# Performance work log

Hardware: AMD Instinct MI355X
Metric: run time of the kernel (lower is better)

Reference implementation:

```python
import jax, jax.numpy as jnp
import numpy as np

N, E, IN_DIM, EDGE_DIM, HID, OUT = 20000, 160000, 128, 32, 128, 64


def _p(key, shape):
    return jax.random.normal(key, shape, dtype=jnp.float32) * 0.05


def setup_inputs() -> dict:
    key = jax.random.key(0)
    ks = jax.random.split(key, 24)
    inp = {
        "x": jax.random.normal(ks[0], (N, IN_DIM), dtype=jnp.float32),
        "ei": jax.random.randint(ks[1], (2, E), 0, N, dtype=jnp.int64),
        "ea": jax.random.normal(ks[2], (E, EDGE_DIM), dtype=jnp.float32),
    }
    H1C1 = 4 * HID  # layer1: heads=4, out=HID, concat -> 512
    # layer 1 params (in=IN_DIM)
    inp["Wq1"] = _p(ks[3], (H1C1, IN_DIM)); inp["bq1"] = _p(ks[4], (H1C1,))
    inp["Wk1"] = _p(ks[5], (H1C1, IN_DIM)); inp["bk1"] = _p(ks[6], (H1C1,))
    inp["Wv1"] = _p(ks[7], (H1C1, IN_DIM)); inp["bv1"] = _p(ks[8], (H1C1,))
    inp["We1"] = _p(ks[9], (H1C1, EDGE_DIM))
    inp["Ws1"] = _p(ks[10], (H1C1, IN_DIM)); inp["bs1"] = _p(ks[11], (H1C1,))
    # layer 2 params (in=512, heads=1, out=OUT, concat=False)
    IN2 = H1C1
    inp["Wq2"] = _p(ks[12], (OUT, IN2)); inp["bq2"] = _p(ks[13], (OUT,))
    inp["Wk2"] = _p(ks[14], (OUT, IN2)); inp["bk2"] = _p(ks[15], (OUT,))
    inp["Wv2"] = _p(ks[16], (OUT, IN2)); inp["bv2"] = _p(ks[17], (OUT,))
    inp["We2"] = _p(ks[18], (OUT, EDGE_DIM))
    inp["Ws2"] = _p(ks[19], (OUT, IN2)); inp["bs2"] = _p(ks[20], (OUT,))
    return inp


def transformer_conv(x, ei, ea, Wq, bq, Wk, bk, Wv, bv, We, Ws, bs, heads, C, concat):
    """PyG TransformerConv: gather -> per-edge attention -> segment softmax -> scatter."""
    n = x.shape[0]
    src, dst = ei[0], ei[1]  # messages flow src -> dst
    q = (x @ Wq.T + bq).reshape(n, heads, C)
    k = (x @ Wk.T + bk).reshape(n, heads, C)
    v = (x @ Wv.T + bv).reshape(n, heads, C)
    e = (ea @ We.T).reshape(-1, heads, C)  # [E,H,C]
    kj = k[src] + e
    vj = v[src] + e
    alpha = jnp.einsum("ehc,ehc->eh", q[dst], kj) / jnp.sqrt(jnp.float32(C))
    # segment softmax over incoming edges of each dst node
    amax = jax.ops.segment_max(alpha, dst, num_segments=n)
    ex = jnp.exp(alpha - amax[dst])
    denom = jax.ops.segment_sum(ex, dst, num_segments=n)
    w = ex / denom[dst]  # [E,H]
    out = jax.ops.segment_sum(vj * w[:, :, None], dst, num_segments=n)  # [N,H,C]
    out = out.reshape(n, heads * C) if concat else out.mean(axis=1)
    return out + x @ Ws.T + bs  # root/skip connection


def reference(x, ei, ea,
              Wq1, bq1, Wk1, bk1, Wv1, bv1, We1, Ws1, bs1,
              Wq2, bq2, Wk2, bk2, Wv2, bv2, We2, Ws2, bs2):
    h = jax.nn.relu(transformer_conv(x, ei, ea, Wq1, bq1, Wk1, bk1, Wv1, bv1,
                                     We1, Ws1, bs1, heads=4, C=HID, concat=True))
    z = transformer_conv(h, ei, ea, Wq2, bq2, Wk2, bk2, Wv2, bv2,
                         We2, Ws2, bs2, heads=1, C=OUT, concat=False)
    return z
```

## Files before the change

### kernel.cpp

```cpp
#include <hip/hip_runtime.h>
#include <hip/hip_bf16.h>
#include <math.h>

#define N_NODES 20000
#define N_EDGES 160000
#define D1 512
#define D2 64
#define Y1W 2176
#define Y2W 288

typedef __attribute__((ext_vector_type(8))) short short8;
typedef __attribute__((ext_vector_type(4))) float floatx4;

__device__ __forceinline__ float bf2f(short u) {
    return __uint_as_float(((unsigned)(unsigned short)u) << 16);
}
__device__ __forceinline__ short f2bf(float f) {
    __hip_bfloat16 h = __float2bfloat16(f);
    return *(short*)&h;
}

__global__ void hist_kernel(const int* __restrict__ ei, int* __restrict__ deg) {
    int e = blockIdx.x * blockDim.x + threadIdx.x;
    if (e < N_EDGES) atomicAdd(&deg[ei[N_EDGES + e]], 1);
}

__global__ void scan_kernel(const int* __restrict__ deg, int* __restrict__ rowptr) {
    const int NT = 1024;
    const int CH = (N_NODES + NT - 1) / NT;
    __shared__ int sums[NT];
    int t = threadIdx.x;
    int base = t * CH;
    int s = 0;
    for (int i = 0; i < CH; ++i) {
        int idx = base + i;
        if (idx < N_NODES) s += deg[idx];
    }
    sums[t] = s;
    __syncthreads();
    for (int off = 1; off < NT; off <<= 1) {
        int v = (t >= off) ? sums[t - off] : 0;
        __syncthreads();
        sums[t] += v;
        __syncthreads();
    }
    int run = (t > 0) ? sums[t - 1] : 0;
    for (int i = 0; i < CH; ++i) {
        int idx = base + i;
        if (idx < N_NODES) {
            rowptr[idx] = run;
            run += deg[idx];
        }
    }
    if (t == NT - 1) rowptr[N_NODES] = sums[NT - 1];
}

__global__ void fill_kernel(const int* __restrict__ ei, const int* __restrict__ rowptr,
                            int* __restrict__ cursor, int* __restrict__ srcs,
                            int* __restrict__ eid) {
    int e = blockIdx.x * blockDim.x + threadIdx.x;
    if (e < N_EDGES) {
        int src = ei[e];
        int dst = ei[N_EDGES + e];
        int p = rowptr[dst] + atomicAdd(&cursor[dst], 1);
        srcs[p] = src;
        eid[p] = e;
    }
}

__global__ void eaperm_kernel(const float* __restrict__ ea, const int* __restrict__ eid,
                              float* __restrict__ eap) {
    int idx = blockIdx.x * 256 + threadIdx.x;
    if (idx >= N_EDGES * 32) return;
    int p = idx >> 5, d = idx & 31;
    eap[idx] = ea[(size_t)eid[p] * 32 + d];
}

__global__ void prep1_kernel(const float* __restrict__ Wq1, const float* __restrict__ bq1,
                             const float* __restrict__ Wk1, const float* __restrict__ bk1,
                             const float* __restrict__ Wv1, const float* __restrict__ bv1,
                             const float* __restrict__ Ws1, const float* __restrict__ bs1,
                             const float* __restrict__ We1,
                             __hip_bfloat16* __restrict__ W1b, float* __restrict__ b1) {
    int j = blockIdx.x, t = threadIdx.x;
    if (j < 2048) {
        int sel = j >> 9, r = j & 511;
        const float* W = sel == 0 ? Wq1 : sel == 1 ? Wk1 : sel == 2 ? Wv1 : Ws1;
        const float* bs = sel == 0 ? bq1 : sel == 1 ? bk1 : sel == 2 ? bv1 : bs1;
        W1b[(size_t)j * 128 + t] = __float2bfloat16(W[(size_t)r * 128 + t]);
        if (t == 0) b1[j] = bs[r];
    } else {
        int hd = j - 2048, h = hd >> 5, d = hd & 31;
        float acc = 0.f;
        for (int c = 0; c < 128; ++c)
            acc += Wq1[(size_t)(h * 128 + c) * 128 + t] * We1[(size_t)(h * 128 + c) * 32 + d];
        W1b[(size_t)j * 128 + t] = __float2bfloat16(acc);
        if (t == 0) {
            float b = 0.f;
            for (int c = 0; c < 128; ++c) b += bq1[h * 128 + c] * We1[(size_t)(h * 128 + c) * 32 + d];
            b1[j] = b;
        }
    }
}

__global__ void prep2_kernel(const float* __restrict__ Wq2, const float* __restrict__ bq2,
                             const float* __restrict__ Wk2, const float* __restrict__ bk2,
                             const float* __restrict__ Wv2, const float* __restrict__ bv2,
                             const float* __restrict__ Ws2, const float* __restrict__ bs2,
                             const float* __restrict__ We2,
                             __hip_bfloat16* __restrict__ W2b, float* __restrict__ b2) {
    int j = blockIdx.x, t = threadIdx.x;
    for (int kk = t; kk < 512; kk += 256) {
        float val;
        if (j < 256) {
            int sel = j >> 6, r = j & 63;
            const float* W = sel == 0 ? Wq2 : sel == 1 ? Wk2 : sel == 2 ? Wv2 : Ws2;
            val = W[(size_t)r * 512 + kk];
        } else {
            int d = j - 256;
            float acc = 0.f;
            for (int c = 0; c < 64; ++c) acc += Wq2[(size_t)c * 512 + kk] * We2[c * 32 + d];
            val = acc;
        }
        W2b[(size_t)j * 512 + kk] = __float2bfloat16(val);
    }
    if (t == 0) {
        if (j < 256) {
            int sel = j >> 6, r = j & 63;
            const float* bs = sel == 0 ? bq2 : sel == 1 ? bk2 : sel == 2 ? bv2 : bs2;
            b2[j] = bs[r];
        } else {
            int d = j - 256;
            float b = 0.f;
            for (int c = 0; c < 64; ++c) b += bq2[c] * We2[c * 32 + d];
            b2[j] = b;
        }
    }
}

template <int K, bool A_F32, bool OUT_BF16>
__global__ __launch_bounds__(256) void gemm_bt(const void* __restrict__ Ap,
                                               const __hip_bfloat16* __restrict__ B,
                                               const float* __restrict__ bias,
                                               void* __restrict__ Cout,
                                               int M, int N, int tiles_n) {
    __shared__ char lds[65536];
    char* ldsA = lds;
    char* ldsB = lds + 32768;
    int tid = threadIdx.x;
    int bm = blockIdx.x / tiles_n, bn = blockIdx.x % tiles_n;
    int w = tid >> 6, lane = tid & 63;
    int wr = (w >> 1) * 64, wc = (w & 1) * 64;
    int lrow = lane & 15, lk = lane >> 4;
    floatx4 acc[4][4] = {};

    for (int kt = 0; kt < K / 128; ++kt) {
        if (kt) __syncthreads();
        #pragma unroll
        for (int it = 0; it < 8; ++it) {
            int s = it * 256 + tid;
            int row = s >> 4, kslot = s & 15;
            int phys = ((kslot ^ (row & 15)) << 4);
            int gr = bm * 128 + row;
            if (gr > M - 1) gr = M - 1;
            short8 va;
            if (A_F32) {
                const float* Af = (const float*)Ap;
                float4 x0 = *(const float4*)(Af + (size_t)gr * K + kt * 128 + kslot * 8);
                float4 x1 = *(const float4*)(Af + (size_t)gr * K + kt * 128 + kslot * 8 + 4);
                va[0] = f2bf(x0.x); va[1] = f2bf(x0.y); va[2] = f2bf(x0.z); va[3] = f2bf(x0.w);
                va[4] = f2bf(x1.x); va[5] = f2bf(x1.y); va[6] = f2bf(x1.z); va[7] = f2bf(x1.w);
            } else {
                const __hip_bfloat16* Ab = (const __hip_bfloat16*)Ap;
                va = *(const short8*)(Ab + (size_t)gr * K + kt * 128 + kslot * 8);
            }
            *(short8*)(ldsA + row * 256 + phys) = va;
            int gc = bn * 128 + row;
            if (gc > N - 1) gc = N - 1;
            short8 vb = *(const short8*)(B + (size_t)gc * K + kt * 128 + kslot * 8);
            *(short8*)(ldsB + row * 256 + phys) = vb;
        }
        __syncthreads();
        #pragma unroll
        for (int ks = 0; ks < 4; ++ks) {
            short8 af[4], bfr[4];
            #pragma unroll
            for (int m = 0; m < 4; ++m) {
                int r = wr + m * 16 + lrow;
                int kslot = ks * 4 + lk;
                af[m] = *(const short8*)(ldsA + r * 256 + ((kslot ^ (r & 15)) << 4));
            }
            #pragma unroll
            for (int n = 0; n < 4; ++n) {
                int c = wc + n * 16 + lrow;
                int kslot = ks * 4 + lk;
                bfr[n] = *(const short8*)(ldsB + c * 256 + ((kslot ^ (c & 15)) << 4));
            }
            #pragma unroll
            for (int m = 0; m < 4; ++m)
                #pragma unroll
                for (int n = 0; n < 4; ++n)
                    acc[m][n] = __builtin_amdgcn_mfma_f32_16x16x32_bf16(af[m], bfr[n], acc[m][n], 0, 0, 0);
        }
    }

    #pragma unroll
    for (int m = 0; m < 4; ++m) {
        #pragma unroll
        for (int j = 0; j < 4; ++j) {
            int r = bm * 128 + wr + m * 16 + lk * 4 + j;
            if (r >= M) continue;
            #pragma unroll
            for (int n = 0; n < 4; ++n) {
                int gc = bn * 128 + wc + n * 16 + lrow;
                if (gc >= N) continue;
                float v = acc[m][n][j] + bias[gc];
                if (OUT_BF16)
                    ((__hip_bfloat16*)Cout)[(size_t)r * N + gc] = __float2bfloat16(v);
                else
                    ((float*)Cout)[(size_t)r * N + gc] = v;
            }
        }
    }
}

__global__ __launch_bounds__(256) void attn1_kernel(
    const __hip_bfloat16* __restrict__ Y1, const float* __restrict__ eap,
    const int* __restrict__ srcs, const int* __restrict__ rowptr,
    const float* __restrict__ We1, __hip_bfloat16* __restrict__ hb) {
    int wid = threadIdx.x >> 6, lane = threadIdx.x & 63;
    int dst = blockIdx.x * 4 + wid;
    if (dst >= N_NODES) return;
    int c0 = lane * 8;
    int hh = lane >> 4;
    int d0 = (lane & 15) * 2;
    const size_t rowb = (size_t)dst * Y1W;
    short8 qv = *(const short8*)(Y1 + rowb + c0);
    float q[8];
    #pragma unroll
    for (int j = 0; j < 8; ++j) q[j] = bf2f(qv[j]);
    const __hip_bfloat16* pp = Y1 + rowb + 2048 + hh * 32 + d0;
    float pA = __bfloat162float(pp[0]);
    float pB = __bfloat162float(pp[1]);

    float acc[8] = {0.f, 0.f, 0.f, 0.f, 0.f, 0.f, 0.f, 0.f};
    float t0 = 0.f, t1 = 0.f, denom = 0.f;
    int beg = rowptr[dst], end = rowptr[dst + 1];

    for (int i = beg; i < end; i += 8) {
        int n = end - i;
        if (n > 8) n = 8;
        int sr[8];
        float2 ff[8];
        short8 kk[8], vv[8];
        #pragma unroll
        for (int j = 0; j < 8; ++j)
            if (j < n) {
                sr[j] = srcs[i + j];
                ff[j] = *(const float2*)(eap + (size_t)(i + j) * 32 + d0);
            }
        #pragma unroll
        for (int j = 0; j < 8; ++j)
            if (j < n) {
                const __hip_bfloat16* rp = Y1 + (size_t)sr[j] * Y1W;
                kk[j] = *(const short8*)(rp + 512 + c0);
                vv[j] = *(const short8*)(rp + 1024 + c0);
            }
        #pragma unroll
        for (int j = 0; j < 8; ++j)
            if (j < n) {
                float s = pA * ff[j].x + pB * ff[j].y;
                #pragma unroll
                for (int c = 0; c < 8; ++c) s += q[c] * bf2f(kk[j][c]);
                s += __shfl_xor(s, 1);
                s += __shfl_xor(s, 2);
                s += __shfl_xor(s, 4);
                s += __shfl_xor(s, 8);
                float wgt = __expf(s * 0.08838834764831845f);
                denom += wgt;
                #pragma unroll
                for (int c = 0; c < 8; ++c) acc[c] += wgt * bf2f(vv[j][c]);
                t0 += wgt * ff[j].x;
                t1 += wgt * ff[j].y;
            }
    }

    float tt[32];
    int gbase = lane & 48;
    #pragma unroll
    for (int d = 0; d < 32; ++d)
        tt[d] = __shfl((d & 1) ? t1 : t0, gbase + (d >> 1));
    float inv = (end > beg) ? 1.f / denom : 0.f;
    short8 sv = *(const short8*)(Y1 + rowb + 1536 + c0);
    short8 hv;
    #pragma unroll
    for (int j = 0; j < 8; ++j) {
        const float4* wr = (const float4*)(We1 + (size_t)(c0 + j) * 32);
        float sum = 0.f;
        #pragma unroll
        for (int d4 = 0; d4 < 8; ++d4) {
            float4 w4 = wr[d4];
            sum += w4.x * tt[d4 * 4] + w4.y * tt[d4 * 4 + 1]
                 + w4.z * tt[d4 * 4 + 2] + w4.w * tt[d4 * 4 + 3];
        }
        float v = (acc[j] + sum) * inv + bf2f(sv[j]);
        hv[j] = f2bf(v > 0.f ? v : 0.f);
    }
    *(short8*)(hb + (size_t)dst * D1 + c0) = hv;
}

__global__ __launch_bounds__(256) void attn2_kernel(
    const __hip_bfloat16* __restrict__ Y2, const float* __restrict__ eap,
    const int* __restrict__ srcs, const int* __restrict__ rowptr,
    const float* __restrict__ We2, float* __restrict__ zout) {
    int wid = threadIdx.x >> 6, lane = threadIdx.x & 63;
    int dst = blockIdx.x * 4 + wid;
    if (dst >= N_NODES) return;
    const size_t rowb = (size_t)dst * Y2W;
    float qv = __bfloat162float(Y2[rowb + lane]);
    float pv = (lane < 32) ? __bfloat162float(Y2[rowb + 256 + lane]) : 0.f;
    float acc = 0.f, t = 0.f, denom = 0.f;
    int beg = rowptr[dst], end = rowptr[dst + 1];

    for (int i = beg; i < end; i += 8) {
        int n = end - i;
        if (n > 8) n = 8;
        int sr[8];
        float ff[8];
        short kb[8], vb[8];
        #pragma unroll
        for (int j = 0; j < 8; ++j)
            if (j < n) {
                sr[j] = srcs[i + j];
                ff[j] = (lane < 32) ? eap[(size_t)(i + j) * 32 + lane] : 0.f;
            }
        #pragma unroll
        for (int j = 0; j < 8; ++j)
            if (j < n) {
                const __hip_bfloat16* rp = Y2 + (size_t)sr[j] * Y2W;
                kb[j] = *(const short*)(rp + 64 + lane);
                vb[j] = *(const short*)(rp + 128 + lane);
            }
        #pragma unroll
        for (int j = 0; j < 8; ++j)
            if (j < n) {
                float s = qv * bf2f(kb[j]) + pv * ff[j];
                s += __shfl_xor(s, 1);
                s += __shfl_xor(s, 2);
                s += __shfl_xor(s, 4);
                s += __shfl_xor(s, 8);
                s += __shfl_xor(s, 16);
                s += __shfl_xor(s, 32);
                float wgt = __expf(s * 0.125f);
                denom += wgt;
                acc += wgt * bf2f(vb[j]);
                t += wgt * ff[j];
            }
    }

    float tt[32];
    #pragma unroll
    for (int d = 0; d < 32; ++d) tt[d] = __shfl(t, d);
    float inv = (end > beg) ? 1.f / denom : 0.f;
    const float4* wr = (const float4*)(We2 + (size_t)lane * 32);
    float sum = 0.f;
    #pragma unroll
    for (int d4 = 0; d4 < 8; ++d4) {
        float4 w4 = wr[d4];
        sum += w4.x * tt[d4 * 4] + w4.y * tt[d4 * 4 + 1]
             + w4.z * tt[d4 * 4 + 2] + w4.w * tt[d4 * 4 + 3];
    }
    zout[(size_t)dst * D2 + lane] =
        (acc + sum) * inv + __bfloat162float(Y2[rowb + 192 + lane]);
}

extern "C" void kernel_launch(void* const* d_in, const int* in_sizes, int n_in,
                              void* d_out, int out_size, void* d_ws, size_t ws_size,
                              hipStream_t stream) {
    const float* x   = (const float*)d_in[0];
    const int*   ei  = (const int*)d_in[1];
    const float* ea  = (const float*)d_in[2];
    const float* Wq1 = (const float*)d_in[3];  const float* bq1 = (const float*)d_in[4];
    const float* Wk1 = (const float*)d_in[5];  const float* bk1 = (const float*)d_in[6];
    const float* Wv1 = (const float*)d_in[7];  const float* bv1 = (const float*)d_in[8];
    const float* We1 = (const float*)d_in[9];
    const float* Ws1 = (const float*)d_in[10]; const float* bs1 = (const float*)d_in[11];
    const float* Wq2 = (const float*)d_in[12]; const float* bq2 = (const float*)d_in[13];
    const float* Wk2 = (const float*)d_in[14]; const float* bk2 = (const float*)d_in[15];
    const float* Wv2 = (const float*)d_in[16]; const float* bv2 = (const float*)d_in[17];
    const float* We2 = (const float*)d_in[18];
    const float* Ws2 = (const float*)d_in[19]; const float* bs2 = (const float*)d_in[20];
    float* zout = (float*)d_out;

    char* wsb = (char*)d_ws;
    size_t off = 0;
    auto alloc = [&](size_t bytes) -> void* {
        void* p = wsb + off;
        off += (bytes + 255) & ~(size_t)255;
        return p;
    };
    __hip_bfloat16* Y1  = (__hip_bfloat16*)alloc((size_t)N_NODES * Y1W * 2);
    __hip_bfloat16* hbb = (__hip_bfloat16*)alloc((size_t)N_NODES * D1 * 2);
    __hip_bfloat16* Y2  = (__hip_bfloat16*)alloc((size_t)N_NODES * Y2W * 2);
    __hip_bfloat16* W1b = (__hip_bfloat16*)alloc((size_t)2176 * 128 * 2);
    float*          b1  = (float*)alloc(2176 * 4);
    __hip_bfloat16* W2b = (__hip_bfloat16*)alloc((size_t)288 * 512 * 2);
    float*          b2  = (float*)alloc(288 * 4);
    int* deg    = (int*)alloc((size_t)N_NODES * 4);
    int* cursor = (int*)alloc((size_t)N_NODES * 4);
    int* rowptr = (int*)alloc((size_t)(N_NODES + 1) * 4);
    int* srcs   = (int*)alloc((size_t)N_EDGES * 4);
    int* eid    = (int*)alloc((size_t)N_EDGES * 4);
    float* eap  = (float*)alloc((size_t)N_EDGES * 32 * 4);

    hipMemsetAsync(deg, 0, (size_t)N_NODES * 4, stream);
    hipMemsetAsync(cursor, 0, (size_t)N_NODES * 4, stream);

    hist_kernel<<<(N_EDGES + 255) / 256, 256, 0, stream>>>(ei, deg);
    scan_kernel<<<1, 1024, 0, stream>>>(deg, rowptr);
    fill_kernel<<<(N_EDGES + 255) / 256, 256, 0, stream>>>(ei, rowptr, cursor, srcs, eid);
    eaperm_kernel<<<(N_EDGES * 32 + 255) / 256, 256, 0, stream>>>(ea, eid, eap);

    prep1_kernel<<<2176, 128, 0, stream>>>(Wq1, bq1, Wk1, bk1, Wv1, bv1, Ws1, bs1,
                                           We1, W1b, b1);
    prep2_kernel<<<288, 256, 0, stream>>>(Wq2, bq2, Wk2, bk2, Wv2, bv2, Ws2, bs2,
                                          We2, W2b, b2);

    int tiles_m = (N_NODES + 127) / 128;
    gemm_bt<128, true, true><<<tiles_m * 17, 256, 0, stream>>>(
        (const void*)x, W1b, b1, (void*)Y1, N_NODES, Y1W, 17);
    attn1_kernel<<<(N_NODES + 3) / 4, 256, 0, stream>>>(Y1, eap, srcs, rowptr, We1, hbb);

    gemm_bt<512, false, true><<<tiles_m * 3, 256, 0, stream>>>(
        (const void*)hbb, W2b, b2, (void*)Y2, N_NODES, Y2W, 3);
    attn2_kernel<<<(N_NODES + 3) / 4, 256, 0, stream>>>(Y2, eap, srcs, rowptr, We2, zout);
}
```

Baseline: 629.2 us.

## Sort destination nodes by degree and split attention work across two waves per node

Adds a counting sort of destination nodes by in-degree, in descending order, so the attention kernels process high-degree nodes first and load stays balanced across waves. Layer-1 attention now uses two wavefronts per node, each covering two heads with 4 channels per lane. This doubles the wave count and cuts per-wave latency. Both attention kernels drop the 8-edge batched prefetch in favour of a simpler 2-edge unrolled loop, which reduces register pressure but also reduces memory-level parallelism per wave. The change also adds three small kernels, two memsets and an extra indirection through dorder.

```diff
diff --git a/kernel.cpp b/kernel.cpp
--- a/kernel.cpp
+++ b/kernel.cpp
@@ -10,6 +10,7 @@
 #define Y2W 288
 
 typedef __attribute__((ext_vector_type(8))) short short8;
+typedef __attribute__((ext_vector_type(4))) short short4v;
 typedef __attribute__((ext_vector_type(4))) float floatx4;
 
 __device__ __forceinline__ float bf2f(short u) {
@@ -74,6 +75,36 @@
     if (idx >= N_EDGES * 32) return;
     int p = idx >> 5, d = idx & 31;
     eap[idx] = ea[(size_t)eid[p] * 32 + d];
+}
+
+__global__ void dsort_hist_kernel(const int* __restrict__ deg, int* __restrict__ bins) {
+    int n = blockIdx.x * 256 + threadIdx.x;
+    if (n < N_NODES) {
+        int b = deg[n]; if (b > 63) b = 63;
+        atomicAdd(&bins[63 - b], 1);
+    }
+}
+
+__global__ void dsort_scan_kernel(const int* __restrict__ bins, int* __restrict__ binstart) {
+    int t = threadIdx.x;
+    int v = bins[t];
+    int s = v;
+    for (int off = 1; off < 64; off <<= 1) {
+        int u = __shfl_up(s, off);
+        if (t >= off) s += u;
+    }
+    binstart[t] = s - v;
+}
+
+__global__ void dsort_scatter_kernel(const int* __restrict__ deg, const int* __restrict__ binstart,
+                                     int* __restrict__ bincur, int* __restrict__ dorder) {
+    int n = blockIdx.x * 256 + threadIdx.x;
+    if (n < N_NODES) {
+        int b = deg[n]; if (b > 63) b = 63;
+        b = 63 - b;
+        int pos = binstart[b] + atomicAdd(&bincur[b], 1);
+        dorder[pos] = n;
+    }
 }
 
 __global__ void prep1_kernel(const float* __restrict__ Wq1, const float* __restrict__ bq1,
@@ -227,74 +258,72 @@
 __global__ __launch_bounds__(256) void attn1_kernel(
     const __hip_bfloat16* __restrict__ Y1, const float* __restrict__ eap,
     const int* __restrict__ srcs, const int* __restrict__ rowptr,
+    const int* __restrict__ dorder,
     const float* __restrict__ We1, __hip_bfloat16* __restrict__ hb) {
     int wid = threadIdx.x >> 6, lane = threadIdx.x & 63;
-    int dst = blockIdx.x * 4 + wid;
-    if (dst >= N_NODES) return;
-    int c0 = lane * 8;
-    int hh = lane >> 4;
-    int d0 = (lane & 15) * 2;
+    int wslot = blockIdx.x * 4 + wid;
+    if (wslot >= 2 * N_NODES) return;
+    int dst = dorder[wslot >> 1];
+    int pair = wslot & 1;
+    int hh = pair * 2 + (lane >> 5);
+    int cloc = (lane & 31) * 4;
+    int c0 = hh * 128 + cloc;
+    int d = lane & 31;
     const size_t rowb = (size_t)dst * Y1W;
-    short8 qv = *(const short8*)(Y1 + rowb + c0);
-    float q[8];
+
+    short4v qv = *(const short4v*)(Y1 + rowb + c0);
+    float q0 = bf2f(qv[0]), q1 = bf2f(qv[1]), q2 = bf2f(qv[2]), q3 = bf2f(qv[3]);
+    float pv = __bfloat162float(Y1[rowb + 2048 + hh * 32 + d]);
+
+    float accv[4] = {0.f, 0.f, 0.f, 0.f};
+    float t = 0.f, denom = 0.f;
+    int beg = rowptr[dst], end = rowptr[dst + 1];
+
+    auto proc = [&](short4v kk, short4v vv, float eav) {
+        float s = q0 * bf2f(kk[0]) + q1 * bf2f(kk[1])
+                + q2 * bf2f(kk[2]) + q3 * bf2f(kk[3]) + pv * eav;
+        s += __shfl_xor(s, 1);
+        s += __shfl_xor(s, 2);
+        s += __shfl_xor(s, 4);
+        s += __shfl_xor(s, 8);
+        s += __shfl_xor(s, 16);
+        float wgt = __expf(s * 0.08838834764831845f);
+        denom += wgt;
+        accv[0] += wgt * bf2f(vv[0]); accv[1] += wgt * bf2f(vv[1]);
+        accv[2] += wgt * bf2f(vv[2]); accv[3] += wgt * bf2f(vv[3]);
+        t += wgt * eav;
+    };
+
+    int i = beg;
+    for (; i + 2 <= end; i += 2) {
+        int sA = srcs[i], sB = srcs[i + 1];
+        const size_t ra = (size_t)sA * Y1W, rb2 = (size_t)sB * Y1W;
+        short4v kA = *(const short4v*)(Y1 + ra + 512 + c0);
+        short4v kB = *(const short4v*)(Y1 + rb2 + 512 + c0);
+        short4v vA = *(const short4v*)(Y1 + ra + 1024 + c0);
+        short4v vB = *(const short4v*)(Y1 + rb2 + 1024 + c0);
+        float eA = eap[(size_t)i * 32 + d];
+        float eB = eap[(size_t)(i + 1) * 32 + d];
+        proc(kA, vA, eA);
+        proc(kB, vB, eB);
+    }
+    if (i < end) {
+        int sA = srcs[i];
+        const size_t ra = (size_t)sA * Y1W;
+        short4v kA = *(const short4v*)(Y1 + ra + 512 + c0);
+        short4v vA = *(const short4v*)(Y1 + ra + 1024 + c0);
+        proc(kA, vA, eap[(size_t)i * 32 + d]);
+    }
+
+    float tt[32];
+    int gbase = lane & 32;
     #pragma unroll
-    for (int j = 0; j < 8; ++j) q[j] = bf2f(qv[j]);
-    const __hip_bfloat16* pp = Y1 + rowb + 2048 + hh * 32 + d0;
-    float pA = __bfloat162float(pp[0]);
-    float pB = __bfloat162float(pp[1]);
-
-    float acc[8] = {0.f, 0.f, 0.f, 0.f, 0.f, 0.f, 0.f, 0.f};
-    float t0 = 0.f, t1 = 0.f, denom = 0.f;
-    int beg = rowptr[dst], end = rowptr[dst + 1];
-
-    for (int i = beg; i < end; i += 8) {
-        int n = end - i;
-        if (n > 8) n = 8;
-        int sr[8];
-        float2 ff[8];
-        short8 kk[8], vv[8];
-        #pragma unroll
-        for (int j = 0; j < 8; ++j)
-            if (j < n) {
-                sr[j] = srcs[i + j];
-                ff[j] = *(const float2*)(eap + (size_t)(i + j) * 32 + d0);
-            }
-        #pragma unroll
-        for (int j = 0; j < 8; ++j)
-            if (j < n) {
-                const __hip_bfloat16* rp = Y1 + (size_t)sr[j] * Y1W;
-                kk[j] = *(const short8*)(rp + 512 + c0);
-                vv[j] = *(const short8*)(rp + 1024 + c0);
-            }
-        #pragma unroll
-        for (int j = 0; j < 8; ++j)
-            if (j < n) {
-                float s = pA * ff[j].x + pB * ff[j].y;
-                #pragma unroll
-                for (int c = 0; c < 8; ++c) s += q[c] * bf2f(kk[j][c]);
-                s += __shfl_xor(s, 1);
-                s += __shfl_xor(s, 2);
-                s += __shfl_xor(s, 4);
-                s += __shfl_xor(s, 8);
-                float wgt = __expf(s * 0.08838834764831845f);
-                denom += wgt;
-                #pragma unroll
-                for (int c = 0; c < 8; ++c) acc[c] += wgt * bf2f(vv[j][c]);
-                t0 += wgt * ff[j].x;
-                t1 += wgt * ff[j].y;
-            }
-    }
-
-    float tt[32];
-    int gbase = lane & 48;
+    for (int dd = 0; dd < 32; ++dd) tt[dd] = __shfl(t, gbase + dd);
+    float inv = (end > beg) ? 1.f / denom : 0.f;
+    short4v sv = *(const short4v*)(Y1 + rowb + 1536 + c0);
+    short4v hv;
     #pragma unroll
-    for (int d = 0; d < 32; ++d)
-        tt[d] = __shfl((d & 1) ? t1 : t0, gbase + (d >> 1));
-    float inv = (end > beg) ? 1.f / denom : 0.f;
-    short8 sv = *(const short8*)(Y1 + rowb + 1536 + c0);
-    short8 hv;
-    #pragma unroll
-    for (int j = 0; j < 8; ++j) {
+    for (int j = 0; j < 4; ++j) {
         const float4* wr = (const float4*)(We1 + (size_t)(c0 + j) * 32);
         float sum = 0.f;
         #pragma unroll
@@ -303,64 +332,65 @@
             sum += w4.x * tt[d4 * 4] + w4.y * tt[d4 * 4 + 1]
                  + w4.z * tt[d4 * 4 + 2] + w4.w * tt[d4 * 4 + 3];
         }
-        float v = (acc[j] + sum) * inv + bf2f(sv[j]);
+        float v = (accv[j] + sum) * inv + bf2f(sv[j]);
         hv[j] = f2bf(v > 0.f ? v : 0.f);
     }
-    *(short8*)(hb + (size_t)dst * D1 + c0) = hv;
+    *(short4v*)(hb + (size_t)dst * D1 + c0) = hv;
 }
 
 __global__ __launch_bounds__(256) void attn2_kernel(
     const __hip_bfloat16* __restrict__ Y2, const float* __restrict__ eap,
     const int* __restrict__ srcs, const int* __restrict__ rowptr,
+    const int* __restrict__ dorder,
     const float* __restrict__ We2, float* __restrict__ zout) {
     int wid = threadIdx.x >> 6, lane = threadIdx.x & 63;
-    int dst = blockIdx.x * 4 + wid;
-    if (dst >= N_NODES) return;
+    int slot = blockIdx.x * 4 + wid;
+    if (slot >= N_NODES) return;
+    int dst = dorder[slot];
     const size_t rowb = (size_t)dst * Y2W;
     float qv = __bfloat162float(Y2[rowb + lane]);
     float pv = (lane < 32) ? __bfloat162float(Y2[rowb + 256 + lane]) : 0.f;
     float acc = 0.f, t = 0.f, denom = 0.f;
     int beg = rowptr[dst], end = rowptr[dst + 1];
 
-    for (int i = beg; i < end; i += 8) {
-        int n = end - i;
-        if (n > 8) n = 8;
-        int sr[8];
-        float ff[8];
-        short kb[8], vb[8];
-        #pragma unroll
-        for (int j = 0; j < 8; ++j)
-            if (j < n) {
-                sr[j] = srcs[i + j];
-                ff[j] = (lane < 32) ? eap[(size_t)(i + j) * 32 + lane] : 0.f;
-            }
-        #pragma unroll
-        for (int j = 0; j < 8; ++j)
-            if (j < n) {
-                const __hip_bfloat16* rp = Y2 + (size_t)sr[j] * Y2W;
-                kb[j] = *(const short*)(rp + 64 + lane);
-                vb[j] = *(const short*)(rp + 128 + lane);
-            }
-        #pragma unroll
-        for (int j = 0; j < 8; ++j)
-            if (j < n) {
-                float s = qv * bf2f(kb[j]) + pv * ff[j];
-                s += __shfl_xor(s, 1);
-                s += __shfl_xor(s, 2);
-                s += __shfl_xor(s, 4);
-                s += __shfl_xor(s, 8);
-                s += __shfl_xor(s, 16);
-                s += __shfl_xor(s, 32);
-                float wgt = __expf(s * 0.125f);
-                denom += wgt;
-                acc += wgt * bf2f(vb[j]);
-                t += wgt * ff[j];
-            }
+    auto proc = [&](short kb, short vb, float eav) {
+        float s = qv * bf2f(kb) + pv * eav;
+        s += __shfl_xor(s, 1);
+        s += __shfl_xor(s, 2);
+        s += __shfl_xor(s, 4);
+        s += __shfl_xor(s, 8);
+        s += __shfl_xor(s, 16);
+        s += __shfl_xor(s, 32);
+        float wgt = __expf(s * 0.125f);
+        denom += wgt;
+        acc += wgt * bf2f(vb);
+        t += wgt * eav;
+    };
+
+    int i = beg;
+    for (; i + 2 <= end; i += 2) {
+        int sA = srcs[i], sB = srcs[i + 1];
+        const size_t ra = (size_t)sA * Y2W, rb2 = (size_t)sB * Y2W;
+        short kA = *(const short*)(Y2 + ra + 64 + lane);
+        short kB = *(const short*)(Y2 + rb2 + 64 + lane);
+        short vA = *(const short*)(Y2 + ra + 128 + lane);
+        short vB = *(const short*)(Y2 + rb2 + 128 + lane);
+        float eA = (lane < 32) ? eap[(size_t)i * 32 + lane] : 0.f;
+        float eB = (lane < 32) ? eap[(size_t)(i + 1) * 32 + lane] : 0.f;
+        proc(kA, vA, eA);
+        proc(kB, vB, eB);
+    }
+    if (i < end) {
+        int sA = srcs[i];
+        const size_t ra = (size_t)sA * Y2W;
+        proc(*(const short*)(Y2 + ra + 64 + lane),
+             *(const short*)(Y2 + ra + 128 + lane),
+             (lane < 32) ? eap[(size_t)i * 32 + lane] : 0.f);
     }
 
     float tt[32];
     #pragma unroll
-    for (int d = 0; d < 32; ++d) tt[d] = __shfl(t, d);
+    for (int dd = 0; dd < 32; ++dd) tt[dd] = __shfl(t, dd);
     float inv = (end > beg) ? 1.f / denom : 0.f;
     const float4* wr = (const float4*)(We2 + (size_t)lane * 32);
     float sum = 0.f;
@@ -412,14 +442,23 @@
     int* srcs   = (int*)alloc((size_t)N_EDGES * 4);
     int* eid    = (int*)alloc((size_t)N_EDGES * 4);
     float* eap  = (float*)alloc((size_t)N_EDGES * 32 * 4);
+    int* bins    = (int*)alloc(64 * 4);
+    int* binstart= (int*)alloc(64 * 4);
+    int* bincur  = (int*)alloc(64 * 4);
+    int* dorder  = (int*)alloc((size_t)N_NODES * 4);
 
     hipMemsetAsync(deg, 0, (size_t)N_NODES * 4, stream);
     hipMemsetAsync(cursor, 0, (size_t)N_NODES * 4, stream);
+    hipMemsetAsync(bins, 0, 64 * 4, stream);
+    hipMemsetAsync(bincur, 0, 64 * 4, stream);
 
     hist_kernel<<<(N_EDGES + 255) / 256, 256, 0, stream>>>(ei, deg);
     scan_kernel<<<1, 1024, 0, stream>>>(deg, rowptr);
     fill_kernel<<<(N_EDGES + 255) / 256, 256, 0, stream>>>(ei, rowptr, cursor, srcs, eid);
     eaperm_kernel<<<(N_EDGES * 32 + 255) / 256, 256, 0, stream>>>(ea, eid, eap);
+    dsort_hist_kernel<<<(N_NODES + 255) / 256, 256, 0, stream>>>(deg, bins);
+    dsort_scan_kernel<<<1, 64, 0, stream>>>(bins, binstart);
+    dsort_scatter_kernel<<<(N_NODES + 255) / 256, 256, 0, stream>>>(deg, binstart, bincur, dorder);
 
     prep1_kernel<<<2176, 128, 0, stream>>>(Wq1, bq1, Wk1, bk1, Wv1, bv1, Ws1, bs1,
                                            We1, W1b, b1);
@@ -429,9 +468,11 @@
     int tiles_m = (N_NODES + 127) / 128;
     gemm_bt<128, true, true><<<tiles_m * 17, 256, 0, stream>>>(
         (const void*)x, W1b, b1, (void*)Y1, N_NODES, Y1W, 17);
-    attn1_kernel<<<(N_NODES + 3) / 4, 256, 0, stream>>>(Y1, eap, srcs, rowptr, We1, hbb);
+    attn1_kernel<<<(2 * N_NODES + 3) / 4, 256, 0, stream>>>(Y1, eap, srcs, rowptr,
+                                                            dorder, We1, hbb);
 
     gemm_bt<512, false, true><<<tiles_m * 3, 256, 0, stream>>>(
         (const void*)hbb, W2b, b2, (void*)Y2, N_NODES, Y2W, 3);
-    attn2_kernel<<<(N_NODES + 3) / 4, 256, 0, stream>>>(Y2, eap, srcs, rowptr, We2, zout);
-}
+    attn2_kernel<<<(N_NODES + 3) / 4, 256, 0, stream>>>(Y2, eap, srcs, rowptr,
+                                                        dorder, We2, zout);
+}
```

After: 734.9 us. 1.17x slower.

## Quantize gathered K/V rows to int8 with per-node scales for attention

Applied to the files above, without the earlier changes.

Adds pack kernels that convert each node's K and V rows to int8 with per-node absmax scales. The attention kernels then gather these compact rows instead of bf16, halving per-edge gather bytes. The edge loop is also restructured from 8-way batching to 2-way unrolling. This costs an extra pack pass per layer, adds quantization error to attention scores and values, and reduces the loads in flight per wave.

```diff
diff --git a/kernel.cpp b/kernel.cpp
--- a/kernel.cpp
+++ b/kernel.cpp
@@ -18,6 +18,14 @@
 __device__ __forceinline__ short f2bf(float f) {
     __hip_bfloat16 h = __float2bfloat16(f);
     return *(short*)&h;
+}
+__device__ __forceinline__ float i8tof(unsigned int u, int c) {
+    return (float)(signed char)((u >> (8 * c)) & 255u);
+}
+__device__ __forceinline__ unsigned int q8(float x, float inv) {
+    float t = x * inv;
+    t = fminf(fmaxf(t, -127.f), 127.f);
+    return (unsigned int)(__float2int_rn(t)) & 255u;
 }
 
 __global__ void hist_kernel(const int* __restrict__ ei, int* __restrict__ deg) {
@@ -138,6 +146,64 @@
     }
 }
 
+__global__ __launch_bounds__(256) void kvpack1_kernel(
+    const __hip_bfloat16* __restrict__ Y1, signed char* __restrict__ KV,
+    float2* __restrict__ sc) {
+    int wid = threadIdx.x >> 6, lane = threadIdx.x & 63;
+    int n = blockIdx.x * 4 + wid;
+    if (n >= N_NODES) return;
+    const __hip_bfloat16* row = Y1 + (size_t)n * Y1W;
+    short8 kv = *(const short8*)(row + 512 + lane * 8);
+    short8 vv = *(const short8*)(row + 1024 + lane * 8);
+    float kf[8], vf[8];
+    float kmax = 0.f, vmax = 0.f;
+    #pragma unroll
+    for (int j = 0; j < 8; ++j) {
+        kf[j] = bf2f(kv[j]); kmax = fmaxf(kmax, fabsf(kf[j]));
+        vf[j] = bf2f(vv[j]); vmax = fmaxf(vmax, fabsf(vf[j]));
+    }
+    #pragma unroll
+    for (int off = 1; off < 64; off <<= 1) {
+        kmax = fmaxf(kmax, __shfl_xor(kmax, off));
+        vmax = fmaxf(vmax, __shfl_xor(vmax, off));
+    }
+    float kinv = kmax > 0.f ? 127.f / kmax : 0.f;
+    float vinv = vmax > 0.f ? 127.f / vmax : 0.f;
+    unsigned int klo = 0, khi = 0, vlo = 0, vhi = 0;
+    #pragma unroll
+    for (int j = 0; j < 4; ++j) {
+        klo |= q8(kf[j], kinv) << (8 * j);
+        khi |= q8(kf[4 + j], kinv) << (8 * j);
+        vlo |= q8(vf[j], vinv) << (8 * j);
+        vhi |= q8(vf[4 + j], vinv) << (8 * j);
+    }
+    *(uint2*)(KV + (size_t)n * 1024 + lane * 8) = make_uint2(klo, khi);
+    *(uint2*)(KV + (size_t)n * 1024 + 512 + lane * 8) = make_uint2(vlo, vhi);
+    if (lane == 0) sc[n] = make_float2(kmax / 127.f, vmax / 127.f);
+}
+
+__global__ __launch_bounds__(256) void kvpack2_kernel(
+    const __hip_bfloat16* __restrict__ Y2, signed char* __restrict__ KV,
+    float2* __restrict__ sc) {
+    int wid = threadIdx.x >> 6, lane = threadIdx.x & 63;
+    int n = blockIdx.x * 4 + wid;
+    if (n >= N_NODES) return;
+    const __hip_bfloat16* row = Y2 + (size_t)n * Y2W;
+    float kf = bf2f(*(const short*)(row + 64 + lane));
+    float vf = bf2f(*(const short*)(row + 128 + lane));
+    float kmax = fabsf(kf), vmax = fabsf(vf);
+    #pragma unroll
+    for (int off = 1; off < 64; off <<= 1) {
+        kmax = fmaxf(kmax, __shfl_xor(kmax, off));
+        vmax = fmaxf(vmax, __shfl_xor(vmax, off));
+    }
+    float kinv = kmax > 0.f ? 127.f / kmax : 0.f;
+    float vinv = vmax > 0.f ? 127.f / vmax : 0.f;
+    KV[(size_t)n * 128 + lane] = (signed char)(q8(kf, kinv));
+    KV[(size_t)n * 128 + 64 + lane] = (signed char)(q8(vf, vinv));
+    if (lane == 0) sc[n] = make_float2(kmax / 127.f, vmax / 127.f);
+}
+
 template <int K, bool A_F32, bool OUT_BF16>
 __global__ __launch_bounds__(256) void gemm_bt(const void* __restrict__ Ap,
                                                const __hip_bfloat16* __restrict__ B,
@@ -225,7 +291,8 @@
 }
 
 __global__ __launch_bounds__(256) void attn1_kernel(
-    const __hip_bfloat16* __restrict__ Y1, const float* __restrict__ eap,
+    const __hip_bfloat16* __restrict__ Y1, const signed char* __restrict__ KV1,
+    const float2* __restrict__ sc1, const float* __restrict__ eap,
     const int* __restrict__ srcs, const int* __restrict__ rowptr,
     const float* __restrict__ We1, __hip_bfloat16* __restrict__ hb) {
     int wid = threadIdx.x >> 6, lane = threadIdx.x & 63;
@@ -247,42 +314,50 @@
     float t0 = 0.f, t1 = 0.f, denom = 0.f;
     int beg = rowptr[dst], end = rowptr[dst + 1];
 
-    for (int i = beg; i < end; i += 8) {
-        int n = end - i;
-        if (n > 8) n = 8;
-        int sr[8];
-        float2 ff[8];
-        short8 kk[8], vv[8];
-        #pragma unroll
-        for (int j = 0; j < 8; ++j)
-            if (j < n) {
-                sr[j] = srcs[i + j];
-                ff[j] = *(const float2*)(eap + (size_t)(i + j) * 32 + d0);
-            }
-        #pragma unroll
-        for (int j = 0; j < 8; ++j)
-            if (j < n) {
-                const __hip_bfloat16* rp = Y1 + (size_t)sr[j] * Y1W;
-                kk[j] = *(const short8*)(rp + 512 + c0);
-                vv[j] = *(const short8*)(rp + 1024 + c0);
-            }
-        #pragma unroll
-        for (int j = 0; j < 8; ++j)
-            if (j < n) {
-                float s = pA * ff[j].x + pB * ff[j].y;
-                #pragma unroll
-                for (int c = 0; c < 8; ++c) s += q[c] * bf2f(kk[j][c]);
-                s += __shfl_xor(s, 1);
-                s += __shfl_xor(s, 2);
-                s += __shfl_xor(s, 4);
-                s += __shfl_xor(s, 8);
-                float wgt = __expf(s * 0.08838834764831845f);
-                denom += wgt;
-                #pragma unroll
-                for (int c = 0; c < 8; ++c) acc[c] += wgt * bf2f(vv[j][c]);
-                t0 += wgt * ff[j].x;
-                t1 += wgt * ff[j].y;
-            }
+    auto proc = [&](uint2 ku, uint2 vu, float2 sc, float ea0, float ea1) {
+        float sdot = 0.f;
+        #pragma unroll
+        for (int c = 0; c < 4; ++c) sdot += q[c] * i8tof(ku.x, c);
+        #pragma unroll
+        for (int c = 0; c < 4; ++c) sdot += q[4 + c] * i8tof(ku.y, c);
+        float s = sdot * sc.x + pA * ea0 + pB * ea1;
+        s += __shfl_xor(s, 1);
+        s += __shfl_xor(s, 2);
+        s += __shfl_xor(s, 4);
+        s += __shfl_xor(s, 8);
+        float wgt = __expf(s * 0.08838834764831845f);
+        denom += wgt;
+        float wv = wgt * sc.y;
+        #pragma unroll
+        for (int c = 0; c < 4; ++c) acc[c] += wv * i8tof(vu.x, c);
+        #pragma unroll
+        for (int c = 0; c < 4; ++c) acc[4 + c] += wv * i8tof(vu.y, c);
+        t0 += wgt * ea0;
+        t1 += wgt * ea1;
+    };
+
+    int i = beg;
+    for (; i + 2 <= end; i += 2) {
+        int sA = srcs[i], sB = srcs[i + 1];
+        const signed char* ka = KV1 + (size_t)sA * 1024 + c0;
+        const signed char* kb = KV1 + (size_t)sB * 1024 + c0;
+        uint2 kA = *(const uint2*)ka;
+        uint2 kB = *(const uint2*)kb;
+        uint2 vA = *(const uint2*)(ka + 512);
+        uint2 vB = *(const uint2*)(kb + 512);
+        float2 scA = sc1[sA], scB = sc1[sB];
+        float2 fA = *(const float2*)(eap + (size_t)i * 32 + d0);
+        float2 fB = *(const float2*)(eap + (size_t)(i + 1) * 32 + d0);
+        proc(kA, vA, scA, fA.x, fA.y);
+        proc(kB, vB, scB, fB.x, fB.y);
+    }
+    if (i < end) {
+        int sA = srcs[i];
+        const signed char* ka = KV1 + (size_t)sA * 1024 + c0;
+        uint2 kA = *(const uint2*)ka;
+        uint2 vA = *(const uint2*)(ka + 512);
+        float2 fA = *(const float2*)(eap + (size_t)i * 32 + d0);
+        proc(kA, vA, sc1[sA], fA.x, fA.y);
     }
 
     float tt[32];
@@ -310,7 +385,8 @@
 }
 
 __global__ __launch_bounds__(256) void attn2_kernel(
-    const __hip_bfloat16* __restrict__ Y2, const float* __restrict__ eap,
+    const __hip_bfloat16* __restrict__ Y2, const signed char* __restrict__ KV2,
+    const float2* __restrict__ sc2, const float* __restrict__ eap,
     const int* __restrict__ srcs, const int* __restrict__ rowptr,
     const float* __restrict__ We2, float* __restrict__ zout) {
     int wid = threadIdx.x >> 6, lane = threadIdx.x & 63;
@@ -322,45 +398,43 @@
     float acc = 0.f, t = 0.f, denom = 0.f;
     int beg = rowptr[dst], end = rowptr[dst + 1];
 
-    for (int i = beg; i < end; i += 8) {
-        int n = end - i;
-        if (n > 8) n = 8;
-        int sr[8];
-        float ff[8];
-        short kb[8], vb[8];
-        #pragma unroll
-        for (int j = 0; j < 8; ++j)
-            if (j < n) {
-                sr[j] = srcs[i + j];
-                ff[j] = (lane < 32) ? eap[(size_t)(i + j) * 32 + lane] : 0.f;
-            }
-        #pragma unroll
-        for (int j = 0; j < 8; ++j)
-            if (j < n) {
-                const __hip_bfloat16* rp = Y2 + (size_t)sr[j] * Y2W;
-                kb[j] = *(const short*)(rp + 64 + lane);
-                vb[j] = *(const short*)(rp + 128 + lane);
-            }
-        #pragma unroll
-        for (int j = 0; j < 8; ++j)
-            if (j < n) {
-                float s = qv * bf2f(kb[j]) + pv * ff[j];
-                s += __shfl_xor(s, 1);
-                s += __shfl_xor(s, 2);
-                s += __shfl_xor(s, 4);
-                s += __shfl_xor(s, 8);
-                s += __shfl_xor(s, 16);
-                s += __shfl_xor(s, 32);
-                float wgt = __expf(s * 0.125f);
-                denom += wgt;
-                acc += wgt * bf2f(vb[j]);
-                t += wgt * ff[j];
-            }
+    auto proc = [&](float kq, float vq, float2 sc, float eav) {
+        float s = qv * kq * sc.x + pv * eav;
+        s += __shfl_xor(s, 1);
+        s += __shfl_xor(s, 2);
+        s += __shfl_xor(s, 4);
+        s += __shfl_xor(s, 8);
+        s += __shfl_xor(s, 16);
+        s += __shfl_xor(s, 32);
+        float wgt = __expf(s * 0.125f);
+        denom += wgt;
+        acc += wgt * sc.y * vq;
+        t += wgt * eav;
+    };
+
+    int i = beg;
+    for (; i + 2 <= end; i += 2) {
+        int sA = srcs[i], sB = srcs[i + 1];
+        const signed char* ra = KV2 + (size_t)sA * 128;
+        const signed char* rb = KV2 + (size_t)sB * 128;
+        float kA = (float)ra[lane], kB = (float)rb[lane];
+        float vA = (float)ra[64 + lane], vB = (float)rb[64 + lane];
+        float2 scA = sc2[sA], scB = sc2[sB];
+        float eA = (lane < 32) ? eap[(size_t)i * 32 + lane] : 0.f;
+        float eB = (lane < 32) ? eap[(size_t)(i + 1) * 32 + lane] : 0.f;
+        proc(kA, vA, scA, eA);
+        proc(kB, vB, scB, eB);
+    }
+    if (i < end) {
+        int sA = srcs[i];
+        const signed char* ra = KV2 + (size_t)sA * 128;
+        proc((float)ra[lane], (float)ra[64 + lane], sc2[sA],
+             (lane < 32) ? eap[(size_t)i * 32 + lane] : 0.f);
     }
 
     float tt[32];
     #pragma unroll
-    for (int d = 0; d < 32; ++d) tt[d] = __shfl(t, d);
+    for (int dd = 0; dd < 32; ++dd) tt[dd] = __shfl(t, dd);
     float inv = (end > beg) ? 1.f / denom : 0.f;
     const float4* wr = (const float4*)(We2 + (size_t)lane * 32);
     float sum = 0.f;
@@ -402,6 +476,10 @@
     __hip_bfloat16* Y1  = (__hip_bfloat16*)alloc((size_t)N_NODES * Y1W * 2);
     __hip_bfloat16* hbb = (__hip_bfloat16*)alloc((size_t)N_NODES * D1 * 2);
     __hip_bfloat16* Y2  = (__hip_bfloat16*)alloc((size_t)N_NODES * Y2W * 2);
+    signed char*    KV1 = (signed char*)alloc((size_t)N_NODES * 1024);
+    float2*         sc1 = (float2*)alloc((size_t)N_NODES * 8);
+    signed char*    KV2 = (signed char*)alloc((size_t)N_NODES * 128);
+    float2*         sc2 = (float2*)alloc((size_t)N_NODES * 8);
     __hip_bfloat16* W1b = (__hip_bfloat16*)alloc((size_t)2176 * 128 * 2);
     float*          b1  = (float*)alloc(2176 * 4);
     __hip_bfloat16* W2b = (__hip_bfloat16*)alloc((size_t)288 * 512 * 2);
@@ -429,9 +507,13 @@
     int tiles_m = (N_NODES + 127) / 128;
     gemm_bt<128, true, true><<<tiles_m * 17, 256, 0, stream>>>(
         (const void*)x, W1b, b1, (void*)Y1, N_NODES, Y1W, 17);
-    attn1_kernel<<<(N_NODES + 3) / 4, 256, 0, stream>>>(Y1, eap, srcs, rowptr, We1, hbb);
+    kvpack1_kernel<<<(N_NODES + 3) / 4, 256, 0, stream>>>(Y1, KV1, sc1);
+    attn1_kernel<<<(N_NODES + 3) / 4, 256, 0, stream>>>(Y1, KV1, sc1, eap, srcs,
+                                                        rowptr, We1, hbb);
 
     gemm_bt<512, false, true><<<tiles_m * 3, 256, 0, stream>>>(
         (const void*)hbb, W2b, b2, (void*)Y2, N_NODES, Y2W, 3);
-    attn2_kernel<<<(N_NODES + 3) / 4, 256, 0, stream>>>(Y2, eap, srcs, rowptr, We2, zout);
-}
+    kvpack2_kernel<<<(N_NODES + 3) / 4, 256, 0, stream>>>(Y2, KV2, sc2);
+    attn2_kernel<<<(N_NODES + 3) / 4, 256, 0, stream>>>(Y2, KV2, sc2, eap, srcs,
+                                                        rowptr, We2, zout);
+}
```

After: 591.8 us. -5.9%, faster.
